# Kernel optimization log

Hardware: AMD Instinct MI355X
Metric: run time of the kernel (lower is better)

Reference implementation:

```python
import jax, jax.numpy as jnp
import numpy as np

B, T, D = 2, 2048, 1024
H, HD = 16, 64
MAX_LEN = 2048


def setup_inputs() -> dict:
    key = jax.random.key(0)
    ks = jax.random.split(key, 7)
    s = 0.02
    return {
        "x": jax.random.normal(ks[0], (B, T, D), dtype=jnp.float32),
        "qkv_w": jax.random.normal(ks[1], (3 * D, D), dtype=jnp.float32) * s,
        "qkv_b": jax.random.normal(ks[2], (3 * D,), dtype=jnp.float32) * s,
        "out_w": jax.random.normal(ks[3], (D, D), dtype=jnp.float32) * s,
        "out_b": jax.random.normal(ks[4], (D,), dtype=jnp.float32) * s,
        "rel_pos": jax.random.normal(ks[5], (2 * MAX_LEN - 1, HD), dtype=jnp.float32),
        "rpe_w": jax.random.normal(ks[6], (HD,), dtype=jnp.float32) * s,
    }


def reference(x, qkv_w, qkv_b, out_w, out_b, rel_pos, rpe_w):
    Bq, Tq, Dq = x.shape
    scale = HD ** -0.5
    qkv = x @ qkv_w.T + qkv_b  # [B,T,3D]
    qkv = qkv.reshape(Bq, Tq, 3, H, HD)
    q = qkv[:, :, 0].transpose(0, 2, 1, 3)  # [B,H,T,HD]
    k = qkv[:, :, 1].transpose(0, 2, 1, 3)
    v = qkv[:, :, 2].transpose(0, 2, 1, 3)
    scores = jnp.einsum('bhqd,bhkd->bhqk', q, k) * scale  # [B,H,T,T]
    # relative position bias: gather rel embeddings, project to scalar
    rel_idx = jnp.arange(Tq)[None, :] - jnp.arange(Tq)[:, None] + MAX_LEN - 1  # [T,T]
    bias = (rel_pos @ rpe_w)[rel_idx]  # project first (cheap), then gather -> [T,T]
    scores = scores + bias[None, None]
    attn = jax.nn.softmax(scores, axis=-1)
    out = jnp.einsum('bhqk,bhkd->bhqd', attn, v)  # [B,H,T,HD]
    out = out.transpose(0, 2, 1, 3).reshape(Bq, Tq, Dq)
    return out @ out_w.T + out_b
```

## Files before the change

kernel.cpp:

```cpp
#include <hip/hip_runtime.h>
#include <math.h>

#define B_ 2
#define T_ 2048
#define D_ 1024
#define H_ 16
#define HD_ 64
#define MAXLEN_ 2048
#define N3D_ 3072
#define M_ (B_ * T_)
#define KA 1024

#define SCALE_L2E 0.18033688011116215f
#define L2E 1.4426950408889634f

typedef unsigned short ushort_t;
typedef __attribute__((ext_vector_type(8))) short short8;
typedef __attribute__((ext_vector_type(4))) float floatx4;
#define MFMA16(a, b, c) __builtin_amdgcn_mfma_f32_16x16x32_bf16(a, b, c, 0, 0, 0)

static __device__ __forceinline__ ushort_t f2bf(float f) {
    unsigned u = __float_as_uint(f);
    unsigned r = (u + 0x7FFFu + ((u >> 16) & 1u)) >> 16;
    return (ushort_t)r;
}
static __device__ __forceinline__ unsigned packrnu(float a, float b) {
    unsigned ua = __float_as_uint(a) + 0x8000u;
    unsigned ub = __float_as_uint(b) + 0x8000u;
    return __builtin_amdgcn_perm(ub, ua, 0x07060302u);
}

static __device__ __forceinline__ void gld16(const ushort_t* g, ushort_t* l) {
    __builtin_amdgcn_global_load_lds(
        (const __attribute__((address_space(1))) void*)g,
        (__attribute__((address_space(3))) void*)l, 16, 0, 0);
}

__global__ __launch_bounds__(256) void cvt_all(
    const float* __restrict__ x, const float* __restrict__ qw,
    const float* __restrict__ ow, const float* __restrict__ rel_pos,
    const float* __restrict__ rpe_w,
    ushort_t* __restrict__ Xc, ushort_t* __restrict__ QWc,
    ushort_t* __restrict__ OWc, float* __restrict__ biasp)
{
    const int row = blockIdx.x;
    if (row < M_ + N3D_ + D_) {
        const float* src; ushort_t* dst; int r;
        if (row < M_)            { src = x;  dst = Xc;  r = row; }
        else if (row < M_ + N3D_){ src = qw; dst = QWc; r = row - M_; }
        else                     { src = ow; dst = OWc; r = row - M_ - N3D_; }
        const int c = threadIdx.x * 4;
        float4 v = *(const float4*)(src + (size_t)r * 1024 + c);
        ushort4 hv;
        hv.x = f2bf(v.x); hv.y = f2bf(v.y); hv.z = f2bf(v.z); hv.w = f2bf(v.w);
        *(ushort4*)(dst + (size_t)r * KA + c) = hv;
    } else {
        const int wv = threadIdx.x >> 6, lane = threadIdx.x & 63;
        const int r = (row - (M_ + N3D_ + D_)) * 4 + wv;
        if (r < 2 * MAXLEN_ - 1) {
            float v = rel_pos[(size_t)r * HD_ + lane] * rpe_w[lane];
#pragma unroll
            for (int off = 32; off; off >>= 1) v += __shfl_down(v, off);
            if (lane == 0) biasp[r] = v * L2E;
        }
    }
}

__global__ __launch_bounds__(512, 2) void qkv_mfma(
    const ushort_t* __restrict__ Ac, const ushort_t* __restrict__ Bc,
    const float* __restrict__ bias,
    ushort_t* __restrict__ Qs, ushort_t* __restrict__ Khi,
    ushort_t* __restrict__ Vt)
{
    __shared__ __align__(16) ushort_t LDS[2][2][32 * 512];

    const int tid = threadIdx.x;
    const int wv = tid >> 6, lane = tid & 63;
    const int l16 = lane & 15, quad = lane >> 4;
    const int wr = wv >> 2, wc = wv & 3;

    const int orig = blockIdx.y * 12 + blockIdx.x;
    const int swz = (orig & 7) * 24 + (orig >> 3);
    const int m0 = (swz / 12) * 256, n0 = (swz % 12) * 256;

    floatx4 acc[8][4];
#pragma unroll
    for (int i = 0; i < 8; ++i)
#pragma unroll
        for (int j = 0; j < 4; ++j) acc[i][j] = (floatx4){0.f, 0.f, 0.f, 0.f};

    short8 af[4][2];
    short8 bf[2][2][2];

#define BARX() asm volatile("s_barrier" ::: "memory")
#define WAITVM(n) asm volatile("s_waitcnt vmcnt(" #n ")" ::: "memory")

#define STAGE(bufi, ab, unit, tile) do {                                      \
    const ushort_t* _src = (ab) ? Bc : Ac;                                    \
    const int _rc = (ab) ? n0 : m0;                                           \
    const int _I = (unit) * 8 + wv;                                           \
    const ushort_t* _g = _src + (size_t)(_rc + _I * 16 + l16) * KA            \
                              + ((tile) * 64 + quad * 8);                     \
    ushort_t* _l = &LDS[bufi][ab][(_I * 2) * 512];                            \
    gld16(_g, _l);                                                            \
    gld16(_g + 32, _l + 512);                                                 \
} while (0)

#define RD_AF(bufi, mi) do {                                                  \
    _Pragma("unroll") for (int ii = 0; ii < 4; ++ii) {                        \
        const int _I = wr * 8 + (mi) * 4 + ii;                                \
        af[ii][0] = *(const short8*)(&LDS[bufi][0][(_I * 2 + 0) * 512] + lane * 8); \
        af[ii][1] = *(const short8*)(&LDS[bufi][0][(_I * 2 + 1) * 512] + lane * 8); \
    } } while (0)

#define RD_BF(bufi, ni) do {                                                  \
    _Pragma("unroll") for (int jj = 0; jj < 2; ++jj) {                        \
        const int _I = wc * 4 + (ni) * 2 + jj;                                \
        bf[ni][jj][0] = *(const short8*)(&LDS[bufi][1][(_I * 2 + 0) * 512] + lane * 8); \
        bf[ni][jj][1] = *(const short8*)(&LDS[bufi][1][(_I * 2 + 1) * 512] + lane * 8); \
    } } while (0)

#define MM(mi, ni) do {                                                       \
    __builtin_amdgcn_s_setprio(1);                                            \
    _Pragma("unroll") for (int ii = 0; ii < 4; ++ii)                          \
    _Pragma("unroll") for (int jj = 0; jj < 2; ++jj) {                        \
        acc[(mi)*4+ii][(ni)*2+jj] = MFMA16(af[ii][0], bf[ni][jj][0], acc[(mi)*4+ii][(ni)*2+jj]); \
        acc[(mi)*4+ii][(ni)*2+jj] = MFMA16(af[ii][1], bf[ni][jj][1], acc[(mi)*4+ii][(ni)*2+jj]); \
    }                                                                         \
    __builtin_amdgcn_s_setprio(0);                                            \
} while (0)

    STAGE(0, 1, 0, 0); STAGE(0, 1, 1, 0);
    STAGE(0, 0, 0, 0); STAGE(0, 0, 1, 0);
    STAGE(1, 1, 0, 1); STAGE(1, 1, 1, 1);
    WAITVM(4);
    BARX();

#pragma unroll 1
    for (int j = 0; j < 8; ++j) {
        const int tY  = 2 * j + 1;
        const int tX2 = (2 * j + 2) & 15;
        const int tY2 = (2 * j + 3) & 15;
        RD_AF(0, 0); RD_BF(0, 0); STAGE(1, 0, 0, tY);  BARX(); MM(0, 0); BARX();
        RD_BF(0, 1);              STAGE(1, 0, 1, tY);  BARX(); MM(0, 1); BARX();
        RD_AF(0, 1);              STAGE(0, 1, 0, tX2); BARX(); MM(1, 0); BARX();
                                  STAGE(0, 1, 1, tX2); BARX(); MM(1, 1);
        WAITVM(4); BARX();
        RD_AF(1, 0); RD_BF(1, 0); STAGE(0, 0, 0, tX2); BARX(); MM(0, 0); BARX();
        RD_BF(1, 1);              STAGE(0, 0, 1, tX2); BARX(); MM(0, 1); BARX();
        RD_AF(1, 1);              STAGE(1, 1, 0, tY2); BARX(); MM(1, 0); BARX();
                                  STAGE(1, 1, 1, tY2); BARX(); MM(1, 1);
        WAITVM(4); BARX();
    }

#undef BARX
#undef WAITVM
#undef STAGE
#undef RD_AF
#undef RD_BF
#undef MM

#pragma unroll
    for (int mi = 0; mi < 8; ++mi) {
#pragma unroll
        for (int r = 0; r < 4; ++r) {
            const int m = m0 + wr * 128 + mi * 16 + quad * 4 + r;
            const int bb = m >> 11, t = m & 2047;
#pragma unroll
            for (int jj = 0; jj < 4; ++jj) {
                const int n = n0 + wc * 64 + jj * 16 + l16;
                const int c = n >> 10, h = (n >> 6) & 15, hd = n & 63;
                const float v = acc[mi][jj][r] + bias[n];
                const size_t idx = (((size_t)bb * H_ + h) * T_ + t) * HD_ + hd;
                if (c == 0) { Qs[idx] = f2bf(v * SCALE_L2E); }
                else if (c == 1) { Khi[idx] = f2bf(v); }
                else { Vt[(((size_t)bb * H_ + h) * HD_ + hd) * T_ + t] = f2bf(v); }
            }
        }
    }
}

__global__ __launch_bounds__(256) void out_mfma(
    const ushort_t* __restrict__ Ac, const ushort_t* __restrict__ Bc,
    const float* __restrict__ bias, float* __restrict__ Out)
{
    __shared__ __align__(16) ushort_t As[2][16 * 512];
    __shared__ __align__(16) ushort_t Bs[2][8 * 512];
    const int tid = threadIdx.x;
    const int wv = tid >> 6, lane = tid & 63;
    const int l16 = lane & 15, quad = lane >> 4;
    const int wm = wv & 1, wn = wv >> 1;

    const int orig = blockIdx.y * 16 + blockIdx.x;
    const int swz = (orig & 7) * 64 + (orig >> 3);
    const int m0 = (swz >> 4) * 128, n0 = (swz & 15) * 64;

    floatx4 acc[4][2];
#pragma unroll
    for (int i = 0; i < 4; ++i)
#pragma unroll
        for (int j = 0; j < 2; ++j) acc[i][j] = (floatx4){0.f, 0.f, 0.f, 0.f};

    auto stage = [&](int bufi, int kk) {
#pragma unroll
        for (int c = 0; c < 4; ++c) {
            const int b = wv * 4 + c;
            const int i = b >> 1, ks = b & 1;
            const int k = kk + ks * 32 + quad * 8;
            gld16(Ac + (size_t)(m0 + i * 16 + l16) * KA + k, As[bufi] + b * 512);
        }
#pragma unroll
        for (int c = 0; c < 2; ++c) {
            const int b = wv * 2 + c;
            const int j = b >> 1, ks = b & 1;
            const int k = kk + ks * 32 + quad * 8;
            gld16(Bc + (size_t)(n0 + j * 16 + l16) * KA + k, Bs[bufi] + b * 512);
        }
    };

    stage(0, 0);
    __syncthreads();

#pragma unroll 1
    for (int t = 0; t < 16; ++t) {
        const int cur = t & 1;
        if (t < 15) stage(cur ^ 1, (t + 1) * 64);
#pragma unroll
        for (int ks = 0; ks < 2; ++ks) {
            short8 af[4], bf[2];
#pragma unroll
            for (int ii = 0; ii < 4; ++ii)
                af[ii] = *(const short8*)(As[cur] + ((wm * 4 + ii) * 2 + ks) * 512 + lane * 8);
#pragma unroll
            for (int jj = 0; jj < 2; ++jj)
                bf[jj] = *(const short8*)(Bs[cur] + ((wn * 2 + jj) * 2 + ks) * 512 + lane * 8);
#pragma unroll
            for (int ii = 0; ii < 4; ++ii)
#pragma unroll
                for (int jj = 0; jj < 2; ++jj)
                    acc[ii][jj] = MFMA16(af[ii], bf[jj], acc[ii][jj]);
        }
        if (t < 15) __syncthreads();
    }

#pragma unroll
    for (int ii = 0; ii < 4; ++ii) {
#pragma unroll
        for (int r = 0; r < 4; ++r) {
            const int m = m0 + wm * 64 + ii * 16 + quad * 4 + r;
#pragma unroll
            for (int jj = 0; jj < 2; ++jj) {
                const int n = n0 + wn * 32 + jj * 16 + l16;
                Out[(size_t)m * D_ + n] = acc[ii][jj][r] + bias[n];
            }
        }
    }
}

#define PSW(x) ((x) ^ ((((x) >> 6) & 1) << 3))

__global__ __launch_bounds__(256) void attn_mfma(
    const ushort_t* __restrict__ Qs, const ushort_t* __restrict__ Khi,
    const ushort_t* __restrict__ Vt, const float* __restrict__ biasp,
    ushort_t* __restrict__ AOc)
{
    __shared__ __align__(16) ushort_t KS[2][8 * 512];
    __shared__ __align__(16) ushort_t VS[2][8 * 512];
    __shared__ __align__(16) ushort_t PS[4][2][1024];

    const int i = blockIdx.x;
    const int j = i >> 3;
    const int bh = (i & 7) + 8 * (j >> 4);
    const int q0 = (j & 15) * 128;
    const int tid = threadIdx.x;
    const int wv = tid >> 6, lane = tid & 63;
    const int l16 = lane & 15, quad = lane >> 4;

    const int qw = q0 + wv * 32;

    short8 qh[2][2];
#pragma unroll
    for (int u = 0; u < 2; ++u) {
        const size_t qoff = ((size_t)bh * T_ + qw + u * 16 + l16) * HD_ + quad * 8;
        qh[u][0] = *(const short8*)(Qs + qoff);
        qh[u][1] = *(const short8*)(Qs + qoff + 32);
    }

    float l_r[2] = {0.f, 0.f};
    floatx4 o_acc[4][2];
#pragma unroll
    for (int g2 = 0; g2 < 4; ++g2)
#pragma unroll
        for (int u = 0; u < 2; ++u) o_acc[g2][u] = (floatx4){0.f, 0.f, 0.f, 0.f};

    const ushort_t* gK = Khi + (size_t)bh * T_ * HD_;
    const ushort_t* gV = Vt + (size_t)bh * HD_ * T_;
    const int c0base = 2047 + quad * 4 - (qw + 16 + l16);
    const int qdbase = quad >> 1;

    const size_t kstage = (size_t)(wv * 16 + l16) * HD_ + quad * 8;
    const size_t vstage = (size_t)(wv * 16 + l16) * T_ + quad * 8;

    gld16(gK + kstage,      KS[0] + (wv * 2 + 0) * 512);
    gld16(gK + kstage + 32, KS[0] + (wv * 2 + 1) * 512);
    gld16(gV + vstage,      VS[0] + (wv * 2 + 0) * 512);
    gld16(gV + vstage + 32, VS[0] + (wv * 2 + 1) * 512);
    __syncthreads();

    for (int t = 0; t < 32; ++t) {
        const int k0 = t * 64;
        const int buf = t & 1, nbuf = buf ^ 1;

        float4 f4[5];
        {
            const float* bp = biasp + (c0base + k0);
#pragma unroll
            for (int z = 0; z < 5; ++z)
                __builtin_memcpy(&f4[z], bp + z * 16, 16);
        }

        if (t < 31) {
            const size_t koff = kstage + (size_t)(k0 + 64) * HD_;
            gld16(gK + koff,      KS[nbuf] + (wv * 2 + 0) * 512);
            gld16(gK + koff + 32, KS[nbuf] + (wv * 2 + 1) * 512);
            const size_t voff = vstage + (size_t)(k0 + 64);
            gld16(gV + voff,      VS[nbuf] + (wv * 2 + 0) * 512);
            gld16(gV + voff + 32, VS[nbuf] + (wv * 2 + 1) * 512);
        }

#pragma unroll
        for (int g = 0; g < 4; ++g) {
            const short8 kh0 = *(const short8*)(KS[buf] + (g * 2 + 0) * 512 + lane * 8);
            const short8 kh1 = *(const short8*)(KS[buf] + (g * 2 + 1) * 512 + lane * 8);
            const int qd = 2 * (g & 1) + qdbase;
#pragma unroll
            for (int u = 0; u < 2; ++u) {
                const float4 bbv = f4[g + 1 - u];
                floatx4 a = (floatx4){bbv.x, bbv.y, bbv.z, bbv.w};
                a = MFMA16(kh0, qh[u][0], a);
                a = MFMA16(kh1, qh[u][1], a);
                const float p0 = __builtin_amdgcn_exp2f(a[0]);
                const float p1 = __builtin_amdgcn_exp2f(a[1]);
                const float p2 = __builtin_amdgcn_exp2f(a[2]);
                const float p3 = __builtin_amdgcn_exp2f(a[3]);
                l_r[u] += (p0 + p1) + (p2 + p3);
                uint2 pkd;
                pkd.x = packrnu(p0, p1);
                pkd.y = packrnu(p2, p3);
                const int widx = (g >> 1) * 512 + (qd * 16 + l16) * 8 + (quad & 1) * 4;
                *(uint2*)(PS[wv][u] + PSW(widx)) = pkd;
            }
        }

        short8 pf[2][2];
#pragma unroll
        for (int u = 0; u < 2; ++u) {
            pf[u][0] = *(const short8*)(PS[wv][u] + PSW(lane * 8));
            pf[u][1] = *(const short8*)(PS[wv][u] + PSW(512 + lane * 8));
        }

#pragma unroll
        for (int g2 = 0; g2 < 4; ++g2) {
            const short8 v0 = *(const short8*)(VS[buf] + (g2 * 2 + 0) * 512 + lane * 8);
            const short8 v1 = *(const short8*)(VS[buf] + (g2 * 2 + 1) * 512 + lane * 8);
#pragma unroll
            for (int u = 0; u < 2; ++u) {
                o_acc[g2][u] = MFMA16(v0, pf[u][0], o_acc[g2][u]);
                o_acc[g2][u] = MFMA16(v1, pf[u][1], o_acc[g2][u]);
            }
        }
        __syncthreads();
    }

    const int bb2 = bh >> 4, h2 = bh & 15;
#pragma unroll
    for (int u = 0; u < 2; ++u) {
        l_r[u] += __shfl_xor(l_r[u], 16);
        l_r[u] += __shfl_xor(l_r[u], 32);
        const float inv = 1.0f / l_r[u];
        const size_t m = (size_t)bb2 * T_ + qw + u * 16 + l16;
#pragma unroll
        for (int g2 = 0; g2 < 4; ++g2) {
            uint2 pk;
            pk.x = packrnu(o_acc[g2][u][0] * inv, o_acc[g2][u][1] * inv);
            pk.y = packrnu(o_acc[g2][u][2] * inv, o_acc[g2][u][3] * inv);
            *(uint2*)(AOc + m * KA + h2 * 64 + g2 * 16 + quad * 4) = pk;
        }
    }
}

extern "C" void kernel_launch(void* const* d_in, const int* in_sizes, int n_in,
                              void* d_out, int out_size, void* d_ws, size_t ws_size,
                              hipStream_t stream)
{
    const float* x       = (const float*)d_in[0];
    const float* qkv_w   = (const float*)d_in[1];
    const float* qkv_b   = (const float*)d_in[2];
    const float* out_w   = (const float*)d_in[3];
    const float* out_b   = (const float*)d_in[4];
    const float* rel_pos = (const float*)d_in[5];
    const float* rpe_w   = (const float*)d_in[6];
    float* out = (float*)d_out;

    const size_t QE = (size_t)B_ * H_ * T_ * HD_;
    ushort_t* Qs  = (ushort_t*)d_ws;
    ushort_t* Khi = Qs  + QE;
    ushort_t* Vt  = Khi + QE;
    ushort_t* Xc  = Vt  + QE;
    ushort_t* QWc = Xc  + (size_t)M_ * KA;
    ushort_t* OWc = QWc + (size_t)N3D_ * KA;
    ushort_t* AOc = OWc + (size_t)D_ * KA;
    float* biasp  = (float*)(AOc + (size_t)M_ * KA);

    cvt_all<<<M_ + N3D_ + D_ + 1024, 256, 0, stream>>>(
        x, qkv_w, out_w, rel_pos, rpe_w, Xc, QWc, OWc, biasp);

    qkv_mfma<<<dim3(12, 16), 512, 0, stream>>>(
        Xc, QWc, qkv_b, Qs, Khi, Vt);
    attn_mfma<<<512, 256, 0, stream>>>(Qs, Khi, Vt, biasp, AOc);
    out_mfma<<<dim3(D_ / 64, M_ / 128), 256, 0, stream>>>(
        AOc, OWc, out_b, out);
}
```

Baseline: 245.5 us.

## Load K/V fragments directly from global into registers, dropping LDS staging

The attention kernel no longer stages K and V tiles through double-buffered shared memory with async loads and per-iteration block barriers. Each wave now reads its K and V MFMA fragments straight from global memory into registers, so all four waves read the same data independently and rely on cache for reuse. Launch bounds now request two blocks per SM and the loop is left un-unrolled. This removes the barrier and LDS traffic but adds redundant global/L2 loads and loses the software prefetch overlap.

```diff
diff --git a/kernel.cpp b/kernel.cpp
--- a/kernel.cpp
+++ b/kernel.cpp
@@ -259,13 +259,11 @@
 
 #define PSW(x) ((x) ^ ((((x) >> 6) & 1) << 3))
 
-__global__ __launch_bounds__(256) void attn_mfma(
+__global__ __launch_bounds__(256, 2) void attn_mfma(
     const ushort_t* __restrict__ Qs, const ushort_t* __restrict__ Khi,
     const ushort_t* __restrict__ Vt, const float* __restrict__ biasp,
     ushort_t* __restrict__ AOc)
 {
-    __shared__ __align__(16) ushort_t KS[2][8 * 512];
-    __shared__ __align__(16) ushort_t VS[2][8 * 512];
     __shared__ __align__(16) ushort_t PS[4][2][1024];
 
     const int i = blockIdx.x;
@@ -293,23 +291,13 @@
 #pragma unroll
         for (int u = 0; u < 2; ++u) o_acc[g2][u] = (floatx4){0.f, 0.f, 0.f, 0.f};
 
-    const ushort_t* gK = Khi + (size_t)bh * T_ * HD_;
-    const ushort_t* gV = Vt + (size_t)bh * HD_ * T_;
+    const ushort_t* kptr = Khi + ((size_t)bh * T_ + l16) * HD_ + quad * 8;
+    const ushort_t* vptr = Vt + (size_t)bh * HD_ * T_ + (size_t)l16 * T_ + quad * 8;
     const int c0base = 2047 + quad * 4 - (qw + 16 + l16);
-    const int qdbase = quad >> 1;
-
-    const size_t kstage = (size_t)(wv * 16 + l16) * HD_ + quad * 8;
-    const size_t vstage = (size_t)(wv * 16 + l16) * T_ + quad * 8;
-
-    gld16(gK + kstage,      KS[0] + (wv * 2 + 0) * 512);
-    gld16(gK + kstage + 32, KS[0] + (wv * 2 + 1) * 512);
-    gld16(gV + vstage,      VS[0] + (wv * 2 + 0) * 512);
-    gld16(gV + vstage + 32, VS[0] + (wv * 2 + 1) * 512);
-    __syncthreads();
-
+
+#pragma unroll 1
     for (int t = 0; t < 32; ++t) {
         const int k0 = t * 64;
-        const int buf = t & 1, nbuf = buf ^ 1;
 
         float4 f4[5];
         {
@@ -319,26 +307,30 @@
                 __builtin_memcpy(&f4[z], bp + z * 16, 16);
         }
 
-        if (t < 31) {
-            const size_t koff = kstage + (size_t)(k0 + 64) * HD_;
-            gld16(gK + koff,      KS[nbuf] + (wv * 2 + 0) * 512);
-            gld16(gK + koff + 32, KS[nbuf] + (wv * 2 + 1) * 512);
-            const size_t voff = vstage + (size_t)(k0 + 64);
-            gld16(gV + voff,      VS[nbuf] + (wv * 2 + 0) * 512);
-            gld16(gV + voff + 32, VS[nbuf] + (wv * 2 + 1) * 512);
-        }
+        short8 kh[4][2];
+#pragma unroll
+        for (int g = 0; g < 4; ++g)
+#pragma unroll
+            for (int dh = 0; dh < 2; ++dh)
+                kh[g][dh] = *(const short8*)(kptr + (size_t)(k0 + g * 16) * HD_ + dh * 32);
+
+        short8 vf[4][2];
+#pragma unroll
+        for (int g2 = 0; g2 < 4; ++g2)
+#pragma unroll
+            for (int ks = 0; ks < 2; ++ks)
+                vf[g2][ks] = *(const short8*)(vptr + (size_t)(g2 * 16) * T_ + k0 + ks * 32);
 
 #pragma unroll
         for (int g = 0; g < 4; ++g) {
-            const short8 kh0 = *(const short8*)(KS[buf] + (g * 2 + 0) * 512 + lane * 8);
-            const short8 kh1 = *(const short8*)(KS[buf] + (g * 2 + 1) * 512 + lane * 8);
-            const int qd = 2 * (g & 1) + qdbase;
+            const int qd = 2 * (g & 1) + (quad >> 1);
+            const int wbase = (g >> 1) * 512 + (qd * 16 + l16) * 8 + (quad & 1) * 4;
 #pragma unroll
             for (int u = 0; u < 2; ++u) {
                 const float4 bbv = f4[g + 1 - u];
                 floatx4 a = (floatx4){bbv.x, bbv.y, bbv.z, bbv.w};
-                a = MFMA16(kh0, qh[u][0], a);
-                a = MFMA16(kh1, qh[u][1], a);
+                a = MFMA16(kh[g][0], qh[u][0], a);
+                a = MFMA16(kh[g][1], qh[u][1], a);
                 const float p0 = __builtin_amdgcn_exp2f(a[0]);
                 const float p1 = __builtin_amdgcn_exp2f(a[1]);
                 const float p2 = __builtin_amdgcn_exp2f(a[2]);
@@ -347,8 +339,7 @@
                 uint2 pkd;
                 pkd.x = packrnu(p0, p1);
                 pkd.y = packrnu(p2, p3);
-                const int widx = (g >> 1) * 512 + (qd * 16 + l16) * 8 + (quad & 1) * 4;
-                *(uint2*)(PS[wv][u] + PSW(widx)) = pkd;
+                *(uint2*)(PS[wv][u] + PSW(wbase)) = pkd;
             }
         }
 
@@ -360,16 +351,12 @@
         }
 
 #pragma unroll
-        for (int g2 = 0; g2 < 4; ++g2) {
-            const short8 v0 = *(const short8*)(VS[buf] + (g2 * 2 + 0) * 512 + lane * 8);
-            const short8 v1 = *(const short8*)(VS[buf] + (g2 * 2 + 1) * 512 + lane * 8);
+        for (int g2 = 0; g2 < 4; ++g2)
 #pragma unroll
             for (int u = 0; u < 2; ++u) {
-                o_acc[g2][u] = MFMA16(v0, pf[u][0], o_acc[g2][u]);
-                o_acc[g2][u] = MFMA16(v1, pf[u][1], o_acc[g2][u]);
+                o_acc[g2][u] = MFMA16(vf[g2][0], pf[u][0], o_acc[g2][u]);
+                o_acc[g2][u] = MFMA16(vf[g2][1], pf[u][1], o_acc[g2][u]);
             }
-        }
-        __syncthreads();
     }
 
     const int bb2 = bh >> 4, h2 = bh & 15;
```

Measured after the change: 304.0 us. +23.8%, slower.
